# Kernel optimization log

Hardware: AMD Instinct MI355X
Metric: run time of the kernel (lower is better)

The kernel has to match this reference:

```python
import jax, jax.numpy as jnp
import numpy as np

D_MODEL = 1280
NUM_HEADS = 16
GROUPS = 5
D_K = D_MODEL // NUM_HEADS  # 80
B, S = 4, 1024


def setup_inputs() -> dict:
    key = jax.random.key(0)
    ks = jax.random.split(key, 12)
    lim_dk = 1.0 / np.sqrt(D_K)
    lim_dm = 1.0 / np.sqrt(D_MODEL)
    return {
        "src": jax.random.normal(ks[0], (B, S, D_MODEL), jnp.float32),
        "k": jax.random.normal(ks[1], (B, S, D_MODEL), jnp.float32),
        "v": jax.random.normal(ks[2], (B, S, D_MODEL), jnp.float32),
        # per-head Linear(d_k, d_k) stacked: weight [H, d_k(out), d_k(in)], bias [H, d_k]
        "Wq": jax.random.uniform(ks[3], (NUM_HEADS, D_K, D_K), jnp.float32, -lim_dk, lim_dk),
        "bq": jax.random.uniform(ks[4], (NUM_HEADS, D_K), jnp.float32, -lim_dk, lim_dk),
        "Wk": jax.random.uniform(ks[5], (NUM_HEADS, D_K, D_K), jnp.float32, -lim_dk, lim_dk),
        "bk": jax.random.uniform(ks[6], (NUM_HEADS, D_K), jnp.float32, -lim_dk, lim_dk),
        "Wv": jax.random.uniform(ks[7], (NUM_HEADS, D_K, D_K), jnp.float32, -lim_dk, lim_dk),
        "bv": jax.random.uniform(ks[8], (NUM_HEADS, D_K), jnp.float32, -lim_dk, lim_dk),
        # output Linear(d_model, d_model)
        "Wo": jax.random.uniform(ks[9], (D_MODEL, D_MODEL), jnp.float32, -lim_dm, lim_dm),
        "bo": jax.random.uniform(ks[10], (D_MODEL,), jnp.float32, -lim_dm, lim_dm),
    }


def reference(src, k, v, Wq, bq, Wk, bk, Wv, bv, Wo, bo):
    # NOTE: original module ignores k, v args; q/k/v all derived from src.
    b, s, d = src.shape
    cpg = d // GROUPS
    # channel shuffle: [B,S,G,C] -> [B,S,C,G] -> [B,S,D]
    x = src.reshape(b, s, GROUPS, cpg).swapaxes(-1, -2).reshape(b, s, d)
    # split heads: [B, H, S, d_k]
    xh = x.reshape(b, s, NUM_HEADS, D_K).transpose(0, 2, 1, 3)
    # per-head distinct linears, batched over heads (torch Linear: x @ W.T + b)
    q = jnp.einsum("bhsd,hed->bhse", xh, Wq) + bq[None, :, None, :]
    kk = jnp.einsum("bhsd,hed->bhse", xh, Wk) + bk[None, :, None, :]
    vv = jnp.einsum("bhsd,hed->bhse", xh, Wv) + bv[None, :, None, :]
    scores = jnp.einsum("bhqd,bhkd->bhqk", q, kk) / jnp.sqrt(jnp.float32(D_K))
    p = jax.nn.softmax(scores, axis=-1)
    heads = jnp.einsum("bhqk,bhkd->bhqd", p, vv)
    concat = heads.transpose(0, 2, 1, 3).reshape(b, s, d)
    return concat @ Wo.T + bo
```

## Files before the change

kernel.cpp:

```cpp
#include <hip/hip_runtime.h>
#include <hip/hip_bf16.h>

#define D_MODEL 1280
#define NUM_HEADS 16
#define D_K 80
#define DP 96
#define SEQ 1024
#define BATCH 4
#define BH (BATCH*NUM_HEADS)

typedef __hip_bfloat16 bf16;
typedef short short8 __attribute__((ext_vector_type(8)));
typedef short short4v __attribute__((ext_vector_type(4)));
typedef float f32x4 __attribute__((ext_vector_type(4)));

__device__ __forceinline__ float b2f(bf16 x) { return __bfloat162float(x); }
__device__ __forceinline__ bf16 f2b(float x) { return __float2bfloat16(x); }
__device__ __forceinline__ short bbits(float x) {
    union { bf16 b; short s; } u; u.b = __float2bfloat16(x); return u.s;
}

#define MFMA16(a, b, c) __builtin_amdgcn_mfma_f32_16x16x32_bf16(a, b, c, 0, 0, 0)

__global__ __launch_bounds__(256) void cvt_all_kernel(
    const float* __restrict__ Wq, const float* __restrict__ Wk,
    const float* __restrict__ Wv, bf16* __restrict__ Wcat,
    const float* __restrict__ Wo, bf16* __restrict__ Wb)
{
    if (blockIdx.x < 1440) {
        int idx = blockIdx.x * 256 + threadIdx.x;
        int col = idx % 96;
        int row = (idx / 96) % 240;
        int h   = idx / (96 * 240);
        int mat = row / 80, e = row % 80;
        int c = col >> 4, j = col & 15;
        const float* W = (mat == 0) ? Wq : (mat == 1) ? Wk : Wv;
        float v = (col < 80) ? W[(size_t)(h * 80 + e) * 80 + (j * 5 + c)] : 0.f;
        Wcat[idx] = f2b(v);
    } else {
        int idx = ((blockIdx.x - 1440) * 256 + threadIdx.x) * 4;
        float4 v = *(const float4*)(Wo + idx);
        Wb[idx]     = f2b(v.x);
        Wb[idx + 1] = f2b(v.y);
        Wb[idx + 2] = f2b(v.z);
        Wb[idx + 3] = f2b(v.w);
    }
}

__global__ __launch_bounds__(256) void qkv_kernel(
    const float* __restrict__ src,
    const float* __restrict__ bq, const float* __restrict__ bk,
    const float* __restrict__ bv, const bf16* __restrict__ Wcat,
    bf16* __restrict__ Qb, bf16* __restrict__ Kb, bf16* __restrict__ Vg)
{
    const int h = blockIdx.y;
    const int b = blockIdx.x >> 3;
    const int s0 = (blockIdx.x & 7) * 128;
    const int tid = threadIdx.x;
    const int wave = tid >> 6, lane = tid & 63;
    const int lquad = lane >> 4, lcol = lane & 15;
    const int bh = b * NUM_HEADS + h;

    short8 xf[2][3];
    #pragma unroll
    for (int mt = 0; mt < 2; mt++)
        #pragma unroll
        for (int ks = 0; ks < 3; ks++) {
            const int c  = 2 * ks + (lquad >> 1);
            const int j0 = (lquad & 1) * 8;
            short8 t = {0, 0, 0, 0, 0, 0, 0, 0};
            if (c < 5) {
                const float* p = src
                    + (size_t)(b * SEQ + s0 + wave * 32 + mt * 16 + lcol) * D_MODEL
                    + c * 256 + h * 16 + j0;
                float4 v0 = *(const float4*)p;
                float4 v1 = *(const float4*)(p + 4);
                t[0] = bbits(v0.x); t[1] = bbits(v0.y);
                t[2] = bbits(v0.z); t[3] = bbits(v0.w);
                t[4] = bbits(v1.x); t[5] = bbits(v1.y);
                t[6] = bbits(v1.z); t[7] = bbits(v1.w);
            }
            xf[mt][ks] = t;
        }

    const bf16* Wh = Wcat + (size_t)h * 240 * 96;
    const float qscale = 1.4426950408889634f * 0.11180339887498949f;
    const f32x4 fzero = {0.f, 0.f, 0.f, 0.f};

    #pragma unroll
    for (int mat = 0; mat < 2; mat++) {
        const bf16* Wm = Wh + mat * 80 * 96;
        short8 wf[5][3];
        #pragma unroll
        for (int n = 0; n < 5; n++)
            #pragma unroll
            for (int ks = 0; ks < 3; ks++)
                wf[n][ks] = *(const short8*)(Wm + (n*16 + lcol)*96 + ks*32 + lquad*8);

        f32x4 acc[2][5];
        #pragma unroll
        for (int n = 0; n < 5; n++) {
            acc[0][n] = MFMA16(xf[0][0], wf[n][0], fzero);
            acc[1][n] = MFMA16(xf[1][0], wf[n][0], fzero);
        }
        #pragma unroll
        for (int ks = 1; ks < 3; ks++)
            #pragma unroll
            for (int n = 0; n < 5; n++) {
                acc[0][n] = MFMA16(xf[0][ks], wf[n][ks], acc[0][n]);
                acc[1][n] = MFMA16(xf[1][ks], wf[n][ks], acc[1][n]);
            }

        const float* bias = (mat == 0) ? bq : bk;
        bf16* Out = (mat == 0) ? Qb : Kb;
        const float scale = (mat == 0) ? qscale : 1.f;
        #pragma unroll
        for (int n = 0; n < 5; n++) {
            float bb = bias[h * 80 + n * 16 + lcol];
            #pragma unroll
            for (int mt = 0; mt < 2; mt++)
                #pragma unroll
                for (int r = 0; r < 4; r++) {
                    int srow = s0 + wave*32 + mt*16 + lquad*4 + r;
                    Out[((size_t)bh * SEQ + srow) * DP + n*16 + lcol] =
                        f2b((acc[mt][n][r] + bb) * scale);
                }
        }
    }
    {
        int i = tid >> 1, half = tid & 1;
        size_t row = ((size_t)bh * SEQ + s0 + i) * DP + 80 + half * 8;
        *(uint4*)(Qb + row) = make_uint4(0, 0, 0, 0);
        *(uint4*)(Kb + row) = make_uint4(0, 0, 0, 0);
    }

    {
        const bf16* Wm = Wh + 2 * 80 * 96;
        short8 wf[5][3];
        #pragma unroll
        for (int m = 0; m < 5; m++)
            #pragma unroll
            for (int ks = 0; ks < 3; ks++)
                wf[m][ks] = *(const short8*)(Wm + (m*16 + lcol)*96 + ks*32 + lquad*8);

        f32x4 acc[5][2];
        #pragma unroll
        for (int m = 0; m < 5; m++) {
            acc[m][0] = MFMA16(wf[m][0], xf[0][0], fzero);
            acc[m][1] = MFMA16(wf[m][0], xf[1][0], fzero);
        }
        #pragma unroll
        for (int ks = 1; ks < 3; ks++)
            #pragma unroll
            for (int m = 0; m < 5; m++) {
                acc[m][0] = MFMA16(wf[m][ks], xf[0][ks], acc[m][0]);
                acc[m][1] = MFMA16(wf[m][ks], xf[1][ks], acc[m][1]);
            }

        #pragma unroll
        for (int m = 0; m < 5; m++) {
            float4 bb4 = *(const float4*)(bv + h * 80 + m * 16 + lquad * 4);
            float bb[4] = {bb4.x, bb4.y, bb4.z, bb4.w};
            #pragma unroll
            for (int nt = 0; nt < 2; nt++)
                #pragma unroll
                for (int r = 0; r < 4; r++) {
                    int e = m*16 + lquad*4 + r;
                    int token = s0 + wave*32 + nt*16 + lcol;
                    Vg[((size_t)bh * D_K + e) * SEQ + token] =
                        f2b(acc[m][nt][r] + bb[r]);
                }
        }
    }
}

__global__ __launch_bounds__(128, 2) void attn_kernel(
    const bf16* __restrict__ Qb, const bf16* __restrict__ Kb,
    const bf16* __restrict__ Vg, bf16* __restrict__ Cc)
{
    __shared__ char smem[26624];
    bf16* Qs = (bf16*)smem;
    bf16* Ks = (bf16*)(smem + 13312);

    const int tid = threadIdx.x;
    const int wave = tid >> 6, lane = tid & 63;
    const int lquad = lane >> 4, lcol = lane & 15;
    const int bh = blockIdx.x;
    const int b = bh >> 4, h = bh & 15;
    const int q0 = blockIdx.y * 64;

    const uint4* Kg = (const uint4*)(Kb + (size_t)bh * SEQ * DP);
    const bf16* Vl = Vg + ((size_t)bh * D_K + lcol) * SEQ + lquad * 8;

    const int i0 = tid, i1 = tid + 128, i2 = tid + 256,
              i3 = tid + 384, i4 = tid + 512, i5 = tid + 640;
    const int kd0 = (i0/12)*104 + (i0%12)*8, kd1 = (i1/12)*104 + (i1%12)*8,
              kd2 = (i2/12)*104 + (i2%12)*8, kd3 = (i3/12)*104 + (i3%12)*8,
              kd4 = (i4/12)*104 + (i4%12)*8, kd5 = (i5/12)*104 + (i5%12)*8;

    {
        const uint4* qg = (const uint4*)(Qb + ((size_t)bh * SEQ + q0) * DP);
        #pragma unroll
        for (int i = 0; i < 6; i++) {
            int idx = tid + i * 128, r = idx / 12, c = idx % 12;
            *(uint4*)(Qs + r * 104 + c * 8) = qg[idx];
        }
    }
    __syncthreads();

    short8 qf[2][3];
    #pragma unroll
    for (int nt = 0; nt < 2; nt++)
        #pragma unroll
        for (int ks = 0; ks < 3; ks++)
            qf[nt][ks] = *(const short8*)(Qs + (wave*32 + nt*16 + lcol)*104 + ks*32 + lquad*8);

    *(uint4*)(Ks + kd0) = Kg[i0];
    *(uint4*)(Ks + kd1) = Kg[i1];
    *(uint4*)(Ks + kd2) = Kg[i2];
    *(uint4*)(Ks + kd3) = Kg[i3];
    *(uint4*)(Ks + kd4) = Kg[i4];
    *(uint4*)(Ks + kd5) = Kg[i5];
    __syncthreads();

    f32x4 Oacc[2][5];
    #pragma unroll
    for (int mt = 0; mt < 2; mt++)
        #pragma unroll
        for (int ne = 0; ne < 5; ne++)
            #pragma unroll
            for (int r = 0; r < 4; r++) Oacc[mt][ne][r] = 0.f;

    f32x4 lsum4[2];
    #pragma unroll
    for (int nt = 0; nt < 2; nt++)
        #pragma unroll
        for (int r = 0; r < 4; r++) lsum4[nt][r] = 0.f;

    bf16* Pw = (bf16*)(smem + wave * 4608);
    const f32x4 fzero = {0.f, 0.f, 0.f, 0.f};

    for (int kt = 0; kt < 16; kt++) {
        const bf16* Vk = Vl + kt * 64;
        short8 v00 = *(const short8*)(Vk);
        short8 v01 = *(const short8*)(Vk + 16 * SEQ);
        short8 v02 = *(const short8*)(Vk + 32 * SEQ);
        short8 v03 = *(const short8*)(Vk + 48 * SEQ);
        short8 v04 = *(const short8*)(Vk + 64 * SEQ);
        short8 v10 = *(const short8*)(Vk + 32);
        short8 v11 = *(const short8*)(Vk + 16 * SEQ + 32);
        short8 v12 = *(const short8*)(Vk + 32 * SEQ + 32);
        short8 v13 = *(const short8*)(Vk + 48 * SEQ + 32);
        short8 v14 = *(const short8*)(Vk + 64 * SEQ + 32);

        const int ktn = (kt + 1) & 15;
        uint4 kA = Kg[ktn * 768 + i0];
        uint4 kB = Kg[ktn * 768 + i1];
        uint4 kC = Kg[ktn * 768 + i2];
        uint4 kD = Kg[ktn * 768 + i3];
        uint4 kE = Kg[ktn * 768 + i4];
        uint4 kF = Kg[ktn * 768 + i5];

        f32x4 st[4][2];
        __builtin_amdgcn_s_setprio(1);
        #pragma unroll
        for (int mt = 0; mt < 4; mt++) {
            short8 af = *(const short8*)(Ks + (mt*16 + lcol)*104 + lquad*8);
            st[mt][0] = MFMA16(af, qf[0][0], fzero);
            st[mt][1] = MFMA16(af, qf[1][0], fzero);
        }
        #pragma unroll
        for (int ks = 1; ks < 3; ks++)
            #pragma unroll
            for (int mt = 0; mt < 4; mt++) {
                short8 af = *(const short8*)(Ks + (mt*16 + lcol)*104 + ks*32 + lquad*8);
                st[mt][0] = MFMA16(af, qf[0][ks], st[mt][0]);
                st[mt][1] = MFMA16(af, qf[1][ks], st[mt][1]);
            }
        __builtin_amdgcn_s_setprio(0);

        #pragma unroll
        for (int nt = 0; nt < 2; nt++)
            #pragma unroll
            for (int mt = 0; mt < 4; mt++) {
                short4v pk;
                #pragma unroll
                for (int r = 0; r < 4; r++) {
                    float p = __builtin_amdgcn_exp2f(st[mt][nt][r]);
                    lsum4[nt][r] += p;
                    pk[r] = bbits(p);
                }
                *(short4v*)(Pw + (nt*16 + lcol)*72 + mt*16 + lquad*4) = pk;
            }

        __builtin_amdgcn_s_setprio(1);
        {
            short8 pf0 = *(const short8*)(Pw + lcol*72 + lquad*8);
            short8 pf1 = *(const short8*)(Pw + (16 + lcol)*72 + lquad*8);
            Oacc[0][0] = MFMA16(pf0, v00, Oacc[0][0]);
            Oacc[1][0] = MFMA16(pf1, v00, Oacc[1][0]);
            Oacc[0][1] = MFMA16(pf0, v01, Oacc[0][1]);
            Oacc[1][1] = MFMA16(pf1, v01, Oacc[1][1]);
            Oacc[0][2] = MFMA16(pf0, v02, Oacc[0][2]);
            Oacc[1][2] = MFMA16(pf1, v02, Oacc[1][2]);
            Oacc[0][3] = MFMA16(pf0, v03, Oacc[0][3]);
            Oacc[1][3] = MFMA16(pf1, v03, Oacc[1][3]);
            Oacc[0][4] = MFMA16(pf0, v04, Oacc[0][4]);
            Oacc[1][4] = MFMA16(pf1, v04, Oacc[1][4]);
        }
        {
            short8 pf0 = *(const short8*)(Pw + lcol*72 + 32 + lquad*8);
            short8 pf1 = *(const short8*)(Pw + (16 + lcol)*72 + 32 + lquad*8);
            Oacc[0][0] = MFMA16(pf0, v10, Oacc[0][0]);
            Oacc[1][0] = MFMA16(pf1, v10, Oacc[1][0]);
            Oacc[0][1] = MFMA16(pf0, v11, Oacc[0][1]);
            Oacc[1][1] = MFMA16(pf1, v11, Oacc[1][1]);
            Oacc[0][2] = MFMA16(pf0, v12, Oacc[0][2]);
            Oacc[1][2] = MFMA16(pf1, v12, Oacc[1][2]);
            Oacc[0][3] = MFMA16(pf0, v13, Oacc[0][3]);
            Oacc[1][3] = MFMA16(pf1, v13, Oacc[1][3]);
            Oacc[0][4] = MFMA16(pf0, v14, Oacc[0][4]);
            Oacc[1][4] = MFMA16(pf1, v14, Oacc[1][4]);
        }
        __builtin_amdgcn_s_setprio(0);

        __syncthreads();
        *(uint4*)(Ks + kd0) = kA;
        *(uint4*)(Ks + kd1) = kB;
        *(uint4*)(Ks + kd2) = kC;
        *(uint4*)(Ks + kd3) = kD;
        *(uint4*)(Ks + kd4) = kE;
        *(uint4*)(Ks + kd5) = kF;
        __syncthreads();
    }

    float inv[2];
    #pragma unroll
    for (int nt = 0; nt < 2; nt++) {
        float s = (lsum4[nt][0] + lsum4[nt][1]) + (lsum4[nt][2] + lsum4[nt][3]);
        s += __shfl_xor(s, 16);
        s += __shfl_xor(s, 32);
        inv[nt] = 1.f / s;
    }
    #pragma unroll
    for (int mt = 0; mt < 2; mt++) {
        f32x4 li;
        #pragma unroll
        for (int r = 0; r < 4; r++)
            li[r] = __shfl(inv[mt], (lane & 48) | (lquad*4 + r));
        #pragma unroll
        for (int ne = 0; ne < 5; ne++)
            #pragma unroll
            for (int r = 0; r < 4; r++) {
                int s_row = q0 + wave*32 + mt*16 + lquad*4 + r;
                int e = ne*16 + lcol;
                Cc[(size_t)(b * SEQ + s_row) * D_MODEL + h * D_K + e] =
                    f2b(Oacc[mt][ne][r] * li[r]);
            }
    }
}

__global__ __launch_bounds__(256) void proj_kernel(
    const bf16* __restrict__ Cc, const bf16* __restrict__ Wb,
    const float* __restrict__ bo, float* __restrict__ out)
{
    __shared__ bf16 As[128 * 72];
    __shared__ bf16 Bs[128 * 72];
    const int tid = threadIdx.x;
    const int wave = tid >> 6, lane = tid & 63;
    const int lquad = lane >> 4, lcol = lane & 15;
    const int t0 = blockIdx.x * 128, o0 = blockIdx.y * 128;
    const int mrow = (wave & 1) * 64, ncol = (wave >> 1) * 64;

    const int i0 = tid, i1 = tid + 256, i2 = tid + 512, i3 = tid + 768;
    const int d0 = (i0>>3)*72 + (i0&7)*8, d1 = (i1>>3)*72 + (i1&7)*8,
              d2 = (i2>>3)*72 + (i2&7)*8, d3 = (i3>>3)*72 + (i3&7)*8;
    const size_t gA0 = (size_t)(t0 + (i0>>3))*D_MODEL + (i0&7)*8;
    const size_t gA1 = (size_t)(t0 + (i1>>3))*D_MODEL + (i1&7)*8;
    const size_t gA2 = (size_t)(t0 + (i2>>3))*D_MODEL + (i2&7)*8;
    const size_t gA3 = (size_t)(t0 + (i3>>3))*D_MODEL + (i3&7)*8;
    const size_t gB0 = (size_t)(o0 + (i0>>3))*D_MODEL + (i0&7)*8;
    const size_t gB1 = (size_t)(o0 + (i1>>3))*D_MODEL + (i1&7)*8;
    const size_t gB2 = (size_t)(o0 + (i2>>3))*D_MODEL + (i2&7)*8;
    const size_t gB3 = (size_t)(o0 + (i3>>3))*D_MODEL + (i3&7)*8;

    *(uint4*)(As + d0) = *(const uint4*)(Cc + gA0);
    *(uint4*)(As + d1) = *(const uint4*)(Cc + gA1);
    *(uint4*)(As + d2) = *(const uint4*)(Cc + gA2);
    *(uint4*)(As + d3) = *(const uint4*)(Cc + gA3);
    *(uint4*)(Bs + d0) = *(const uint4*)(Wb + gB0);
    *(uint4*)(Bs + d1) = *(const uint4*)(Wb + gB1);
    *(uint4*)(Bs + d2) = *(const uint4*)(Wb + gB2);
    *(uint4*)(Bs + d3) = *(const uint4*)(Wb + gB3);
    __syncthreads();

    f32x4 acc[4][4];
    #pragma unroll
    for (int mt = 0; mt < 4; mt++)
        #pragma unroll
        for (int nt = 0; nt < 4; nt++)
            #pragma unroll
            for (int r = 0; r < 4; r++) acc[mt][nt][r] = 0.f;

    for (int kc = 0; kc < 20; kc++) {
        const int kn = (kc < 19) ? (kc + 1) * 64 : 0;
        uint4 pa0 = *(const uint4*)(Cc + gA0 + kn);
        uint4 pa1 = *(const uint4*)(Cc + gA1 + kn);
        uint4 pa2 = *(const uint4*)(Cc + gA2 + kn);
        uint4 pa3 = *(const uint4*)(Cc + gA3 + kn);
        uint4 pb0 = *(const uint4*)(Wb + gB0 + kn);
        uint4 pb1 = *(const uint4*)(Wb + gB1 + kn);
        uint4 pb2 = *(const uint4*)(Wb + gB2 + kn);
        uint4 pb3 = *(const uint4*)(Wb + gB3 + kn);

        __builtin_amdgcn_s_setprio(1);
        #pragma unroll
        for (int ks = 0; ks < 2; ks++) {
            short8 am[4], bn[4];
            #pragma unroll
            for (int t = 0; t < 4; t++) {
                am[t] = *(const short8*)(As + (mrow + t*16 + lcol)*72 + ks*32 + lquad*8);
                bn[t] = *(const short8*)(Bs + (ncol + t*16 + lcol)*72 + ks*32 + lquad*8);
            }
            #pragma unroll
            for (int mt = 0; mt < 4; mt++)
                #pragma unroll
                for (int nt = 0; nt < 4; nt++)
                    acc[mt][nt] = MFMA16(am[mt], bn[nt], acc[mt][nt]);
        }
        __builtin_amdgcn_s_setprio(0);

        __syncthreads();
        *(uint4*)(As + d0) = pa0;
        *(uint4*)(As + d1) = pa1;
        *(uint4*)(As + d2) = pa2;
        *(uint4*)(As + d3) = pa3;
        *(uint4*)(Bs + d0) = pb0;
        *(uint4*)(Bs + d1) = pb1;
        *(uint4*)(Bs + d2) = pb2;
        *(uint4*)(Bs + d3) = pb3;
        __syncthreads();
    }

    #pragma unroll
    for (int nt = 0; nt < 4; nt++) {
        float bias = bo[o0 + ncol + nt*16 + lcol];
        #pragma unroll
        for (int mt = 0; mt < 4; mt++)
            #pragma unroll
            for (int r = 0; r < 4; r++)
                out[(size_t)(t0 + mrow + mt*16 + lquad*4 + r) * D_MODEL
                    + o0 + ncol + nt*16 + lcol] = acc[mt][nt][r] + bias;
    }
}

extern "C" void kernel_launch(void* const* d_in, const int* in_sizes, int n_in,
                              void* d_out, int out_size, void* d_ws, size_t ws_size,
                              hipStream_t stream) {
    const float* src = (const float*)d_in[0];
    const float* Wq = (const float*)d_in[3];
    const float* bq = (const float*)d_in[4];
    const float* Wk = (const float*)d_in[5];
    const float* bk = (const float*)d_in[6];
    const float* Wv = (const float*)d_in[7];
    const float* bv = (const float*)d_in[8];
    const float* Wo = (const float*)d_in[9];
    const float* bo = (const float*)d_in[10];
    float* out = (float*)d_out;

    char* ws = (char*)d_ws;
    bf16* Qb = (bf16*)(ws);
    bf16* Kb = (bf16*)(ws + (size_t)12582912);
    bf16* Vg = (bf16*)(ws + (size_t)25165824);
    bf16* Cc = (bf16*)(ws + (size_t)35651584);
    bf16* Wcat = (bf16*)(ws + (size_t)35651584);
    bf16* Wb = (bf16*)(ws + (size_t)46137344);

    cvt_all_kernel<<<dim3(3040), 256, 0, stream>>>(Wq, Wk, Wv, Wcat, Wo, Wb);
    qkv_kernel<<<dim3(BATCH * SEQ / 128, NUM_HEADS), 256, 0, stream>>>(
        src, bq, bk, bv, Wcat, Qb, Kb, Vg);
    attn_kernel<<<dim3(BH, SEQ / 64), 128, 0, stream>>>(Qb, Kb, Vg, Cc);
    proj_kernel<<<dim3(SEQ * BATCH / 128, D_MODEL / 128), 256, 0, stream>>>(
        Cc, Wb, bo, out);
}
```

Before: 206.6 us.

## Double-buffer K in LDS, keep P in registers, pre-swizzle V layout

The V projection now writes V in a tile-swizzled layout, so each lane's MFMA B-fragments for a 64-key tile sit in contiguous 512-element chunks. The attention kernel double-buffers K in shared memory, which removes one barrier per iteration. Q fragments are loaded straight from global memory instead of being staged through LDS. The softmax probabilities are packed directly into MFMA A-operand registers instead of round-tripping through LDS, relying on the score accumulator layout matching the operand layout. This trades the LDS and barrier traffic for index arithmetic and a layout dependency between the two kernels.

```diff
diff --git a/kernel.cpp b/kernel.cpp
--- a/kernel.cpp
+++ b/kernel.cpp
@@ -165,10 +165,16 @@
             for (int nt = 0; nt < 2; nt++)
                 #pragma unroll
                 for (int r = 0; r < 4; r++) {
-                    int e = m*16 + lquad*4 + r;
-                    int token = s0 + wave*32 + nt*16 + lcol;
-                    Vg[((size_t)bh * D_K + e) * SEQ + token] =
-                        f2b(acc[m][nt][r] + bb[r]);
+                    int elow  = lquad * 4 + r;
+                    int token = s0 + wave * 32 + nt * 16 + lcol;
+                    int kt  = token >> 6;
+                    int js  = (token >> 5) & 1;
+                    int jj  = ((token >> 4) & 1) * 4 + (token & 3);
+                    int lqs = (token >> 2) & 3;
+                    size_t el = (size_t)bh * 81920
+                              + (size_t)((kt * 2 + js) * 5 + m) * 512
+                              + elow * 32 + lqs * 8 + jj;
+                    Vg[el] = f2b(acc[m][nt][r] + bb[r]);
                 }
         }
     }
@@ -179,8 +185,8 @@
     const bf16* __restrict__ Vg, bf16* __restrict__ Cc)
 {
     __shared__ char smem[26624];
-    bf16* Qs = (bf16*)smem;
-    bf16* Ks = (bf16*)(smem + 13312);
+    bf16* Ks0 = (bf16*)smem;
+    bf16* Ks1 = (bf16*)(smem + 13312);
 
     const int tid = threadIdx.x;
     const int wave = tid >> 6, lane = tid & 63;
@@ -190,7 +196,7 @@
     const int q0 = blockIdx.y * 64;
 
     const uint4* Kg = (const uint4*)(Kb + (size_t)bh * SEQ * DP);
-    const bf16* Vl = Vg + ((size_t)bh * D_K + lcol) * SEQ + lquad * 8;
+    const bf16* Vb = Vg + (size_t)bh * 81920 + lcol * 32 + lquad * 8;
 
     const int i0 = tid, i1 = tid + 128, i2 = tid + 256,
               i3 = tid + 384, i4 = tid + 512, i5 = tid + 640;
@@ -198,60 +204,54 @@
               kd2 = (i2/12)*104 + (i2%12)*8, kd3 = (i3/12)*104 + (i3%12)*8,
               kd4 = (i4/12)*104 + (i4%12)*8, kd5 = (i5/12)*104 + (i5%12)*8;
 
-    {
-        const uint4* qg = (const uint4*)(Qb + ((size_t)bh * SEQ + q0) * DP);
-        #pragma unroll
-        for (int i = 0; i < 6; i++) {
-            int idx = tid + i * 128, r = idx / 12, c = idx % 12;
-            *(uint4*)(Qs + r * 104 + c * 8) = qg[idx];
-        }
-    }
+    short8 qf[2][3];
+    #pragma unroll
+    for (int nt = 0; nt < 2; nt++)
+        #pragma unroll
+        for (int ks = 0; ks < 3; ks++)
+            qf[nt][ks] = *(const short8*)(
+                Qb + ((size_t)bh * SEQ + q0 + wave*32 + nt*16 + lcol) * DP
+                   + ks*32 + lquad*8);
+
+    *(uint4*)(Ks0 + kd0) = Kg[i0];
+    *(uint4*)(Ks0 + kd1) = Kg[i1];
+    *(uint4*)(Ks0 + kd2) = Kg[i2];
+    *(uint4*)(Ks0 + kd3) = Kg[i3];
+    *(uint4*)(Ks0 + kd4) = Kg[i4];
+    *(uint4*)(Ks0 + kd5) = Kg[i5];
     __syncthreads();
 
-    short8 qf[2][3];
+    f32x4 Oacc[2][5];
+    #pragma unroll
+    for (int mt = 0; mt < 2; mt++)
+        #pragma unroll
+        for (int ne = 0; ne < 5; ne++)
+            #pragma unroll
+            for (int r = 0; r < 4; r++) Oacc[mt][ne][r] = 0.f;
+
+    f32x4 lsum4[2];
     #pragma unroll
     for (int nt = 0; nt < 2; nt++)
         #pragma unroll
-        for (int ks = 0; ks < 3; ks++)
-            qf[nt][ks] = *(const short8*)(Qs + (wave*32 + nt*16 + lcol)*104 + ks*32 + lquad*8);
-
-    *(uint4*)(Ks + kd0) = Kg[i0];
-    *(uint4*)(Ks + kd1) = Kg[i1];
-    *(uint4*)(Ks + kd2) = Kg[i2];
-    *(uint4*)(Ks + kd3) = Kg[i3];
-    *(uint4*)(Ks + kd4) = Kg[i4];
-    *(uint4*)(Ks + kd5) = Kg[i5];
-    __syncthreads();
-
-    f32x4 Oacc[2][5];
-    #pragma unroll
-    for (int mt = 0; mt < 2; mt++)
-        #pragma unroll
-        for (int ne = 0; ne < 5; ne++)
-            #pragma unroll
-            for (int r = 0; r < 4; r++) Oacc[mt][ne][r] = 0.f;
-
-    f32x4 lsum4[2];
-    #pragma unroll
-    for (int nt = 0; nt < 2; nt++)
-        #pragma unroll
         for (int r = 0; r < 4; r++) lsum4[nt][r] = 0.f;
 
-    bf16* Pw = (bf16*)(smem + wave * 4608);
     const f32x4 fzero = {0.f, 0.f, 0.f, 0.f};
 
     for (int kt = 0; kt < 16; kt++) {
-        const bf16* Vk = Vl + kt * 64;
+        const bf16* cur = (kt & 1) ? Ks1 : Ks0;
+        bf16*       nxt = (kt & 1) ? Ks0 : Ks1;
+
+        const bf16* Vk = Vb + (size_t)kt * 5120;
         short8 v00 = *(const short8*)(Vk);
-        short8 v01 = *(const short8*)(Vk + 16 * SEQ);
-        short8 v02 = *(const short8*)(Vk + 32 * SEQ);
-        short8 v03 = *(const short8*)(Vk + 48 * SEQ);
-        short8 v04 = *(const short8*)(Vk + 64 * SEQ);
-        short8 v10 = *(const short8*)(Vk + 32);
-        short8 v11 = *(const short8*)(Vk + 16 * SEQ + 32);
-        short8 v12 = *(const short8*)(Vk + 32 * SEQ + 32);
-        short8 v13 = *(const short8*)(Vk + 48 * SEQ + 32);
-        short8 v14 = *(const short8*)(Vk + 64 * SEQ + 32);
+        short8 v01 = *(const short8*)(Vk + 512);
+        short8 v02 = *(const short8*)(Vk + 1024);
+        short8 v03 = *(const short8*)(Vk + 1536);
+        short8 v04 = *(const short8*)(Vk + 2048);
+        short8 v10 = *(const short8*)(Vk + 2560);
+        short8 v11 = *(const short8*)(Vk + 3072);
+        short8 v12 = *(const short8*)(Vk + 3584);
+        short8 v13 = *(const short8*)(Vk + 4096);
+        short8 v14 = *(const short8*)(Vk + 4608);
 
         const int ktn = (kt + 1) & 15;
         uint4 kA = Kg[ktn * 768 + i0];
@@ -265,7 +265,7 @@
         __builtin_amdgcn_s_setprio(1);
         #pragma unroll
         for (int mt = 0; mt < 4; mt++) {
-            short8 af = *(const short8*)(Ks + (mt*16 + lcol)*104 + lquad*8);
+            short8 af = *(const short8*)(cur + (mt*16 + lcol)*104 + lquad*8);
             st[mt][0] = MFMA16(af, qf[0][0], fzero);
             st[mt][1] = MFMA16(af, qf[1][0], fzero);
         }
@@ -273,30 +273,26 @@
         for (int ks = 1; ks < 3; ks++)
             #pragma unroll
             for (int mt = 0; mt < 4; mt++) {
-                short8 af = *(const short8*)(Ks + (mt*16 + lcol)*104 + ks*32 + lquad*8);
+                short8 af = *(const short8*)(cur + (mt*16 + lcol)*104 + ks*32 + lquad*8);
                 st[mt][0] = MFMA16(af, qf[0][ks], st[mt][0]);
                 st[mt][1] = MFMA16(af, qf[1][ks], st[mt][1]);
             }
         __builtin_amdgcn_s_setprio(0);
 
-        #pragma unroll
-        for (int nt = 0; nt < 2; nt++)
-            #pragma unroll
-            for (int mt = 0; mt < 4; mt++) {
-                short4v pk;
+        {
+            short8 pf0, pf1;
+            #pragma unroll
+            for (int half = 0; half < 2; half++)
                 #pragma unroll
                 for (int r = 0; r < 4; r++) {
-                    float p = __builtin_amdgcn_exp2f(st[mt][nt][r]);
-                    lsum4[nt][r] += p;
-                    pk[r] = bbits(p);
+                    float p0 = __builtin_amdgcn_exp2f(st[half][0][r]);
+                    float p1 = __builtin_amdgcn_exp2f(st[half][1][r]);
+                    lsum4[0][r] += p0;
+                    lsum4[1][r] += p1;
+                    pf0[half*4+r] = bbits(p0);
+                    pf1[half*4+r] = bbits(p1);
                 }
-                *(short4v*)(Pw + (nt*16 + lcol)*72 + mt*16 + lquad*4) = pk;
-            }
-
-        __builtin_amdgcn_s_setprio(1);
-        {
-            short8 pf0 = *(const short8*)(Pw + lcol*72 + lquad*8);
-            short8 pf1 = *(const short8*)(Pw + (16 + lcol)*72 + lquad*8);
+            __builtin_amdgcn_s_setprio(1);
             Oacc[0][0] = MFMA16(pf0, v00, Oacc[0][0]);
             Oacc[1][0] = MFMA16(pf1, v00, Oacc[1][0]);
             Oacc[0][1] = MFMA16(pf0, v01, Oacc[0][1]);
@@ -307,10 +303,22 @@
             Oacc[1][3] = MFMA16(pf1, v03, Oacc[1][3]);
             Oacc[0][4] = MFMA16(pf0, v04, Oacc[0][4]);
             Oacc[1][4] = MFMA16(pf1, v04, Oacc[1][4]);
+            __builtin_amdgcn_s_setprio(0);
         }
         {
-            short8 pf0 = *(const short8*)(Pw + lcol*72 + 32 + lquad*8);
-            short8 pf1 = *(const short8*)(Pw + (16 + lcol)*72 + 32 + lquad*8);
+            short8 pf0, pf1;
+            #pragma unroll
+            for (int half = 0; half < 2; half++)
+                #pragma unroll
+                for (int r = 0; r < 4; r++) {
+                    float p0 = __builtin_amdgcn_exp2f(st[2+half][0][r]);
+                    float p1 = __builtin_amdgcn_exp2f(st[2+half][1][r]);
+                    lsum4[0][r] += p0;
+                    lsum4[1][r] += p1;
+                    pf0[half*4+r] = bbits(p0);
+                    pf1[half*4+r] = bbits(p1);
+                }
+            __builtin_amdgcn_s_setprio(1);
             Oacc[0][0] = MFMA16(pf0, v10, Oacc[0][0]);
             Oacc[1][0] = MFMA16(pf1, v10, Oacc[1][0]);
             Oacc[0][1] = MFMA16(pf0, v11, Oacc[0][1]);
@@ -321,16 +329,15 @@
             Oacc[1][3] = MFMA16(pf1, v13, Oacc[1][3]);
             Oacc[0][4] = MFMA16(pf0, v14, Oacc[0][4]);
             Oacc[1][4] = MFMA16(pf1, v14, Oacc[1][4]);
-        }
-        __builtin_amdgcn_s_setprio(0);
-
-        __syncthreads();
-        *(uint4*)(Ks + kd0) = kA;
-        *(uint4*)(Ks + kd1) = kB;
-        *(uint4*)(Ks + kd2) = kC;
-        *(uint4*)(Ks + kd3) = kD;
-        *(uint4*)(Ks + kd4) = kE;
-        *(uint4*)(Ks + kd5) = kF;
+            __builtin_amdgcn_s_setprio(0);
+        }
+
+        *(uint4*)(nxt + kd0) = kA;
+        *(uint4*)(nxt + kd1) = kB;
+        *(uint4*)(nxt + kd2) = kC;
+        *(uint4*)(nxt + kd3) = kD;
+        *(uint4*)(nxt + kd4) = kE;
+        *(uint4*)(nxt + kd5) = kF;
         __syncthreads();
     }
 
```

Result: faster. 187.6 us (-9.2%).
